# Kernel tuning notes

Hardware: AMD Instinct MI355X
Metric: run time of the kernel (lower is better)

Reference implementation:

```python
import jax, jax.numpy as jnp
import numpy as np

BATCH = 4096
NUM_INPUTS = 784
WIDTH = 16000        # neurons per logic layer, divisible by NUM_CLASSES
N_HIDDEN = 4         # width->width layers stacked for scan (plus the input layer)
NUM_CLASSES = 10


def setup_inputs() -> dict:
    key = jax.random.key(0)
    ks = jax.random.split(key, 7)
    x = jax.random.bernoulli(ks[0], 0.5, (BATCH, NUM_INPUTS))
    idx_a0 = jax.random.randint(ks[1], (WIDTH,), 0, NUM_INPUTS, dtype=jnp.int32)
    idx_b0 = jax.random.randint(ks[2], (WIDTH,), 0, NUM_INPUTS, dtype=jnp.int32)
    neg0 = jax.random.bernoulli(ks[3], 0.5, (WIDTH, 2))
    idx_a = jax.random.randint(ks[4], (N_HIDDEN, WIDTH), 0, WIDTH, dtype=jnp.int32)
    idx_b = jax.random.randint(ks[5], (N_HIDDEN, WIDTH), 0, WIDTH, dtype=jnp.int32)
    neg = jax.random.bernoulli(ks[6], 0.5, (N_HIDDEN, WIDTH, 2))
    return {"x": x, "idx_a0": idx_a0, "idx_b0": idx_b0, "neg0": neg0,
            "idx_a": idx_a, "idx_b": idx_b, "neg": neg}


def _gate(a, b, nf):
    # gate = (maybe-NOT a) AND (maybe-NOT b); NOT on booleans == XOR with flag
    return (a ^ nf[:, 0]) & (b ^ nf[:, 1])


def reference(x, idx_a0, idx_b0, neg0, idx_a, idx_b, neg):
    # input layer: gather wires from the boolean input
    h = _gate(x[:, idx_a0], x[:, idx_b0], neg0)  # [BATCH, WIDTH] bool

    def step(h, p):
        ia, ib, nf = p
        return _gate(h[:, ia], h[:, ib], nf), None

    h, _ = jax.lax.scan(step, h, (idx_a, idx_b, neg))
    # GroupSum: popcount per class group -> int32 logits
    out = h.reshape(BATCH, NUM_CLASSES, WIDTH // NUM_CLASSES).sum(-1, dtype=jnp.int32)
    return out
```

## Files before the change

### kernel.cpp

```cpp
#include <hip/hip_runtime.h>


#define NIN   784
#define WIDTH 16000
#define SW    16384
#define NH    4
#define NC    10
#define GPC   1600
#define NBLK  128
#define TPB   1024
#define SSTR  13

typedef unsigned int u32;

__global__ void desc_kernel(const int* __restrict__ ia0, const int* __restrict__ ib0,
                            const int* __restrict__ n0,
                            const int* __restrict__ ia, const int* __restrict__ ib,
                            const int* __restrict__ n, u32* __restrict__ desc) {
    int t = blockIdx.x * blockDim.x + threadIdx.x;
    if (t >= (NH + 1) * SW) return;
    int l = t >> 14;
    int g = t & (SW - 1);
    u32 d = 0;
    if (g < WIDTH) {
        int a, b, na, nb;
        if (l == 0) { a = ia0[g]; b = ib0[g]; na = n0[2 * g]; nb = n0[2 * g + 1]; }
        else {
            int o = (l - 1) * WIDTH + g;
            a = ia[o]; b = ib[o]; na = n[2 * o]; nb = n[2 * o + 1];
        }
        d = (u32)a | ((u32)b << 14) | (na ? (1u << 28) : 0u) | (nb ? (1u << 29) : 0u);
    }
    desc[t] = d;
}

__launch_bounds__(TPB)
__global__ void net_kernel(const int* __restrict__ x, const u32* __restrict__ desc,
                           int* __restrict__ out) {
    __shared__ __align__(16) u32 xw[NIN];
    __shared__ __align__(16) u32 bufA[SW];
    __shared__ __align__(16) u32 bufB[SW];

    int w = blockIdx.x;
    int t = threadIdx.x;

    uint4 dreg[4];
    {
        const uint4* d0 = (const uint4*)desc;
#pragma unroll
        for (int j = 0; j < 4; ++j) dreg[j] = d0[t + j * TPB];
    }

    if (t < NIN) {
        const int* base = x + (size_t)(w * 32) * NIN + t;
        u32 acc = 0;
#pragma unroll
        for (int r = 0; r < 32; ++r)
            acc |= (base[(size_t)r * NIN] != 0 ? 1u : 0u) << r;
        xw[t] = acc;
    }
    __syncthreads();

    u32* cur = xw;
#pragma unroll
    for (int l = 0; l <= NH; ++l) {
        u32* dst = (l & 1) ? bufB : bufA;
        uint4 dn[4];
        if (l < NH) {
            const uint4* dq = (const uint4*)(desc + (size_t)(l + 1) * SW);
#pragma unroll
            for (int j = 0; j < 4; ++j) dn[j] = dq[t + j * TPB];
        }
#pragma unroll
        for (int j = 0; j < 4; ++j) {
            u32 d0 = dreg[j].x, d1 = dreg[j].y, d2 = dreg[j].z, d3 = dreg[j].w;
            u32 a0 = cur[d0 & 0x3FFFu], b0 = cur[(d0 >> 14) & 0x3FFFu];
            u32 a1 = cur[d1 & 0x3FFFu], b1 = cur[(d1 >> 14) & 0x3FFFu];
            u32 a2 = cur[d2 & 0x3FFFu], b2 = cur[(d2 >> 14) & 0x3FFFu];
            u32 a3 = cur[d3 & 0x3FFFu], b3 = cur[(d3 >> 14) & 0x3FFFu];
            uint4 r;
            r.x = (a0 ^ (0u - ((d0 >> 28) & 1u))) & (b0 ^ (0u - ((d0 >> 29) & 1u)));
            r.y = (a1 ^ (0u - ((d1 >> 28) & 1u))) & (b1 ^ (0u - ((d1 >> 29) & 1u)));
            r.z = (a2 ^ (0u - ((d2 >> 28) & 1u))) & (b2 ^ (0u - ((d2 >> 29) & 1u)));
            r.w = (a3 ^ (0u - ((d3 >> 28) & 1u))) & (b3 ^ (0u - ((d3 >> 29) & 1u)));
            *(uint4*)(dst + 4 * (t + j * TPB)) = r;
        }
        __syncthreads();
#pragma unroll
        for (int j = 0; j < 4; ++j) dreg[j] = dn[j];
        cur = dst;
    }
    u32* res = bufA;
    u32* scratch = bufB;

    if (t < NC * 100) {
        int c = t / 100, j = t % 100;
        u32 p[12];
#pragma unroll
        for (int q = 0; q < 12; ++q) p[q] = 0;
#pragma unroll
        for (int k = 0; k < 16; ++k) {
            u32 carry = res[c * GPC + k * 100 + j];
#pragma unroll
            for (int q = 0; q < 5; ++q) { u32 s = p[q]; p[q] = s ^ carry; carry = s & carry; }
        }
        u32* sp = scratch + (c * 100 + j) * SSTR;
#pragma unroll
        for (int q = 0; q < 12; ++q) sp[q] = p[q];
    }

    const int widths[5] = {100, 25, 7, 2, 1};
    for (int s = 0; s < 4; ++s) {
        int W = widths[s], Wo = widths[s + 1];
        u32 p[12];
        bool act = (t < NC * Wo);
        int c = 0, j = 0;
        __syncthreads();
        if (act) {
            c = t / Wo; j = t % Wo;
            const u32* pa = scratch + (c * 100 + 4 * j) * SSTR;
#pragma unroll
            for (int q = 0; q < 12; ++q) p[q] = pa[q];
#pragma unroll
            for (int k = 1; k < 4; ++k) {
                if (4 * j + k < W) {
                    const u32* pb = scratch + (c * 100 + 4 * j + k) * SSTR;
                    u32 carry = 0;
#pragma unroll
                    for (int q = 0; q < 12; ++q) {
                        u32 a = p[q], b = pb[q];
                        u32 xr = a ^ b;
                        p[q] = xr ^ carry;
                        carry = (a & b) | (carry & xr);
                    }
                }
            }
        }
        __syncthreads();
        if (act) {
            u32* po = scratch + (c * 100 + j) * SSTR;
#pragma unroll
            for (int q = 0; q < 12; ++q) po[q] = p[q];
        }
    }
    __syncthreads();

    if (t < NC * 32) {
        int c = t / 32, bit = t % 32;
        const u32* sp = scratch + (c * 100) * SSTR;
        int cnt = 0;
#pragma unroll
        for (int q = 0; q < 12; ++q) cnt += (int)((sp[q] >> bit) & 1u) << q;
        out[((size_t)w * 32 + bit) * NC + c] = cnt;
    }
}

extern "C" void kernel_launch(void* const* d_in, const int* in_sizes, int n_in,
                              void* d_out, int out_size, void* d_ws, size_t ws_size,
                              hipStream_t stream) {
    const int* x      = (const int*)d_in[0];
    const int* idx_a0 = (const int*)d_in[1];
    const int* idx_b0 = (const int*)d_in[2];
    const int* neg0   = (const int*)d_in[3];
    const int* idx_a  = (const int*)d_in[4];
    const int* idx_b  = (const int*)d_in[5];
    const int* neg    = (const int*)d_in[6];
    int* out = (int*)d_out;

    u32* desc = (u32*)d_ws;

    int ndesc = (NH + 1) * SW;
    desc_kernel<<<(ndesc + 255) / 256, 256, 0, stream>>>(
        idx_a0, idx_b0, neg0, idx_a, idx_b, neg, desc);

    net_kernel<<<NBLK, TPB, 0, stream>>>(x, desc, out);
}
```

Before: 87.53 us.

## Balance LDS bank conflicts by swapping gate operands; wave-shuffle popcount reduction

Adds a preprocessing kernel that greedily swaps each gate's a/b operands so the two gathered reads in each wavefront spread across shared-memory banks, aiming to cut LDS bank conflicts in the gather loop. It also replaces the multi-stage shared-memory carry-save popcount tree, with its barriers, by per-wave carry-save accumulation followed by cross-lane shuffle adds. The cost is an extra small serial kernel launch per call, and the balancing heuristic may only help partially.

```diff
diff --git a/kernel.cpp b/kernel.cpp
--- a/kernel.cpp
+++ b/kernel.cpp
@@ -9,7 +9,6 @@
 #define GPC   1600
 #define NBLK  128
 #define TPB   1024
-#define SSTR  13
 
 typedef unsigned int u32;
 
@@ -32,6 +31,42 @@
         d = (u32)a | ((u32)b << 14) | (na ? (1u << 28) : 0u) | (nb ? (1u << 29) : 0u);
     }
     desc[t] = d;
+}
+
+#define BAL_TPB 256
+__global__ void balance_kernel(u32* __restrict__ desc) {
+    int u = blockIdx.x * blockDim.x + threadIdx.x;
+    if (u >= 5 * 16 * 4 * 4) return;
+    int e  = u & 3;
+    int j  = (u >> 2) & 3;
+    int w0 = (u >> 4) & 15;
+    int l  = u >> 8;
+    __shared__ u32 cnt[BAL_TPB][16];
+    u32* cA = cnt[threadIdx.x];
+    u32* cB = cnt[threadIdx.x] + 8;
+#pragma unroll
+    for (int q = 0; q < 16; ++q) cnt[threadIdx.x][q] = 0;
+    u32* dp = desc + (size_t)l * SW;
+    for (int L = 0; L < 64; ++L) {
+        int g = 4 * (w0 * 64 + L + 1024 * j) + e;
+        u32 d = dp[g];
+        u32 a = d & 0x3FFFu, b = (d >> 14) & 0x3FFFu;
+        int ba = (int)(a & 31u), bb = (int)(b & 31u);
+        u32 nAa = (cA[ba >> 3] >> ((ba & 7) * 4)) & 15u;
+        u32 nBb = (cB[bb >> 3] >> ((bb & 7) * 4)) & 15u;
+        u32 nAb = (cA[bb >> 3] >> ((bb & 7) * 4)) & 15u;
+        u32 nBa = (cB[ba >> 3] >> ((ba & 7) * 4)) & 15u;
+        u32 costN = (nAa > nBb ? nAa : nBb) * 16u + nAa + nBb;
+        u32 costS = (nAb > nBa ? nAb : nBa) * 16u + nAb + nBa;
+        if (costS < costN) {
+            u32 na = (d >> 28) & 1u, nb = (d >> 29) & 1u;
+            d = b | (a << 14) | (nb << 28) | (na << 29);
+            dp[g] = d;
+            int tm = ba; ba = bb; bb = tm;
+        }
+        if (((cA[ba >> 3] >> ((ba & 7) * 4)) & 15u) < 15u) cA[ba >> 3] += 1u << ((ba & 7) * 4);
+        if (((cB[bb >> 3] >> ((bb & 7) * 4)) & 15u) < 15u) cB[bb >> 3] += 1u << ((bb & 7) * 4);
+    }
 }
 
 __launch_bounds__(TPB)
@@ -91,67 +126,51 @@
         cur = dst;
     }
     u32* res = bufA;
-    u32* scratch = bufB;
 
-    if (t < NC * 100) {
-        int c = t / 100, j = t % 100;
-        u32 p[12];
+    int wave = t >> 6, lane = t & 63;
+    if (wave < NC) {
+        int c = wave;
+        const u32* base = res + c * GPC;
+        u32 p0 = 0, p1 = 0, p2 = 0, p3 = 0, p4 = 0;
+#define CSA5(VAL) { u32 cy = (VAL); u32 s; \
+        s = p0; p0 = s ^ cy; cy = s & cy; \
+        s = p1; p1 = s ^ cy; cy = s & cy; \
+        s = p2; p2 = s ^ cy; cy = s & cy; \
+        s = p3; p3 = s ^ cy; cy = s & cy; \
+        s = p4; p4 = s ^ cy; }
 #pragma unroll
-        for (int q = 0; q < 12; ++q) p[q] = 0;
+        for (int k = 0; k < 6; ++k) {
+            uint4 v = *(const uint4*)(base + 4 * lane + 256 * k);
+            CSA5(v.x); CSA5(v.y); CSA5(v.z); CSA5(v.w);
+        }
+        CSA5(base[1536 + lane]);
+#undef CSA5
+
+        u32 pl[11];
+        pl[0] = p0; pl[1] = p1; pl[2] = p2; pl[3] = p3; pl[4] = p4;
 #pragma unroll
-        for (int k = 0; k < 16; ++k) {
-            u32 carry = res[c * GPC + k * 100 + j];
+        for (int s = 0; s < 6; ++s) {
+            int np = 5 + s;
+            u32 q[11];
 #pragma unroll
-            for (int q = 0; q < 5; ++q) { u32 s = p[q]; p[q] = s ^ carry; carry = s & carry; }
+            for (int i = 0; i < 11; ++i) if (i < np) q[i] = __shfl_xor(pl[i], 1 << s, 64);
+            u32 carry = 0;
+#pragma unroll
+            for (int i = 0; i < 11; ++i) if (i < np) {
+                u32 a = pl[i], b = q[i];
+                u32 xr = a ^ b;
+                pl[i] = xr ^ carry;
+                carry = (a & b) | (carry & xr);
+            }
+            pl[np] = carry;
         }
-        u32* sp = scratch + (c * 100 + j) * SSTR;
+
+        if (lane < 32) {
+            int cntv = 0;
 #pragma unroll
-        for (int q = 0; q < 12; ++q) sp[q] = p[q];
-    }
-
-    const int widths[5] = {100, 25, 7, 2, 1};
-    for (int s = 0; s < 4; ++s) {
-        int W = widths[s], Wo = widths[s + 1];
-        u32 p[12];
-        bool act = (t < NC * Wo);
-        int c = 0, j = 0;
-        __syncthreads();
-        if (act) {
-            c = t / Wo; j = t % Wo;
-            const u32* pa = scratch + (c * 100 + 4 * j) * SSTR;
-#pragma unroll
-            for (int q = 0; q < 12; ++q) p[q] = pa[q];
-#pragma unroll
-            for (int k = 1; k < 4; ++k) {
-                if (4 * j + k < W) {
-                    const u32* pb = scratch + (c * 100 + 4 * j + k) * SSTR;
-                    u32 carry = 0;
-#pragma unroll
-                    for (int q = 0; q < 12; ++q) {
-                        u32 a = p[q], b = pb[q];
-                        u32 xr = a ^ b;
-                        p[q] = xr ^ carry;
-                        carry = (a & b) | (carry & xr);
-                    }
-                }
-            }
+            for (int i = 0; i < 11; ++i) cntv += (int)((pl[i] >> lane) & 1u) << i;
+            out[((size_t)w * 32 + lane) * NC + c] = cntv;
         }
-        __syncthreads();
-        if (act) {
-            u32* po = scratch + (c * 100 + j) * SSTR;
-#pragma unroll
-            for (int q = 0; q < 12; ++q) po[q] = p[q];
-        }
-    }
-    __syncthreads();
-
-    if (t < NC * 32) {
-        int c = t / 32, bit = t % 32;
-        const u32* sp = scratch + (c * 100) * SSTR;
-        int cnt = 0;
-#pragma unroll
-        for (int q = 0; q < 12; ++q) cnt += (int)((sp[q] >> bit) & 1u) << q;
-        out[((size_t)w * 32 + bit) * NC + c] = cnt;
     }
 }
 
@@ -173,5 +192,8 @@
     desc_kernel<<<(ndesc + 255) / 256, 256, 0, stream>>>(
         idx_a0, idx_b0, neg0, idx_a, idx_b, neg, desc);
 
+    int nbal = 5 * 16 * 4 * 4;
+    balance_kernel<<<(nbal + BAL_TPB - 1) / BAL_TPB, BAL_TPB, 0, stream>>>(desc);
+
     net_kernel<<<NBLK, TPB, 0, stream>>>(x, desc, out);
 }
```

Result: slower. 110.5 us (+26.3%).
